# Kernel tuning notes

Measured on AMD Instinct MI355X. Metric: run time of the kernel, lower is better.

Reference implementation:

```python
import jax, jax.numpy as jnp
import numpy as np

B, S, D, H = 2, 2048, 1024, 16
DK = D // H


def setup_inputs() -> dict:
    key = jax.random.key(0)
    ks = jax.random.split(key, 8)
    Q = jax.random.normal(ks[0], (B, S, D), dtype=jnp.float32)
    K = jax.random.normal(ks[1], (B, S, D), dtype=jnp.float32)
    V = jax.random.normal(ks[2], (B, S, D), dtype=jnp.float32)
    scale = 0.02
    W_q = jax.random.normal(ks[3], (D, D), dtype=jnp.float32) * scale
    W_k = jax.random.normal(ks[4], (D, D), dtype=jnp.float32) * scale
    W_v = jax.random.normal(ks[5], (D, D), dtype=jnp.float32) * scale
    W_o = jax.random.normal(ks[6], (D, D), dtype=jnp.float32) * scale
    b_q = jnp.zeros((D,), jnp.float32)
    b_k = jnp.zeros((D,), jnp.float32)
    b_v = jnp.zeros((D,), jnp.float32)
    b_o = jnp.zeros((D,), jnp.float32)
    # causal mask, broadcastable [1,1,S,S]; mask==0 positions are masked out
    mask = jnp.tril(jnp.ones((S, S), jnp.int32))[None, None, :, :]
    return dict(Q=Q, K=K, V=V, W_q=W_q, b_q=b_q, W_k=W_k, b_k=b_k,
                W_v=W_v, b_v=b_v, W_o=W_o, b_o=b_o, mask=mask)


def reference(Q, K, V, W_q, b_q, W_k, b_k, W_v, b_v, W_o, b_o, mask):
    # linear projections (torch Linear equivalent up to weight layout)
    q = Q @ W_q + b_q   # [B,S,D]
    k = K @ W_k + b_k
    v = V @ W_v + b_v
    # split heads -> [B,H,S,DK]
    q = q.reshape(B, S, H, DK).transpose(0, 2, 1, 3)
    k = k.reshape(B, S, H, DK).transpose(0, 2, 1, 3)
    v = v.reshape(B, S, H, DK).transpose(0, 2, 1, 3)
    # scaled dot-product attention with explicit [B,H,S,S] scores
    scores = jnp.einsum('bhqd,bhkd->bhqk', q, k) / jnp.sqrt(jnp.float32(DK))
    scores = jnp.where(mask == 0, jnp.float32(-1e9), scores)
    attn = jax.nn.softmax(scores, axis=-1)
    out = jnp.einsum('bhqk,bhkd->bhqd', attn, v)
    # merge heads and output projection
    out = out.transpose(0, 2, 1, 3).reshape(B, S, D)
    return out @ W_o + b_o
```

## Files before the change

### kernel.cpp

```cpp
#include <hip/hip_runtime.h>


typedef unsigned short u16;
typedef __attribute__((ext_vector_type(8))) short s8v;
typedef __attribute__((ext_vector_type(4))) float f4v;

#define S_ 2048
#define D_ 1024
#define H_ 16
#define DK_ 64

__device__ __forceinline__ u16 f2bf(float f) {
  unsigned u = __builtin_bit_cast(unsigned, f);
  u += 0x7fffu + ((u >> 16) & 1u);
  return (u16)(u >> 16);
}
__device__ __forceinline__ u16 f2bf_t(float f) {
  return (u16)(__builtin_bit_cast(unsigned, f) >> 16);
}

__device__ __forceinline__ void gld_lds16(const u16* g, u16* l) {
  __builtin_amdgcn_global_load_lds(
      (const __attribute__((address_space(1))) unsigned int*)g,
      (__attribute__((address_space(3))) unsigned int*)l, 16, 0, 0);
}

__global__ __launch_bounds__(256) void prep(
    const float* __restrict__ Q, const float* __restrict__ K, const float* __restrict__ V,
    u16* __restrict__ Qc, u16* __restrict__ Kc, u16* __restrict__ Vc,
    const float* __restrict__ W0, const float* __restrict__ W1,
    const float* __restrict__ W2, const float* __restrict__ W3,
    u16* __restrict__ T0, u16* __restrict__ T1, u16* __restrict__ T2, u16* __restrict__ T3) {
  int bid = blockIdx.x, tid = threadIdx.x;
  if (bid < 3072) {
    int z = bid >> 10, t = bid & 1023;
    const float* s = z == 0 ? Q : z == 1 ? K : V;
    u16*         d = z == 0 ? Qc : z == 1 ? Kc : Vc;
    const int n4 = (2 * S_ * D_) / 4;
    for (int idx = t * 256 + tid; idx < n4; idx += 1024 * 256) {
      float4 f = ((const float4*)s)[idx];
      unsigned lo = (unsigned)f2bf(f.x) | ((unsigned)f2bf(f.y) << 16);
      unsigned hi = (unsigned)f2bf(f.z) | ((unsigned)f2bf(f.w) << 16);
      ((uint2*)d)[idx] = make_uint2(lo, hi);
    }
  } else {
    int wb = bid - 3072;
    int z = wb >> 10, t = wb & 1023;
    const float* W = z == 0 ? W0 : z == 1 ? W1 : z == 2 ? W2 : W3;
    u16*         T = z == 0 ? T0 : z == 1 ? T1 : z == 2 ? T2 : T3;
    __shared__ float tile[32][33];
    int tx = tid & 31, ty = tid >> 5;
    int c0 = (t & 31) * 32, r0 = (t >> 5) * 32;
#pragma unroll
    for (int i = 0; i < 32; i += 8)
      tile[ty + i][tx] = W[(size_t)(r0 + ty + i) * D_ + c0 + tx];
    __syncthreads();
#pragma unroll
    for (int i = 0; i < 32; i += 8)
      T[(size_t)(c0 + ty + i) * D_ + r0 + tx] = f2bf(tile[tx][ty + i]);
  }
}

#define BK_ 64

template <int MI, int NJ, int MODE>
__device__ __forceinline__ void gemm_core(const u16* __restrict__ A, const u16* __restrict__ Bt,
                                          const float* __restrict__ bias, void* __restrict__ out,
                                          float oscale, u16* lds, int m0, int n0) {
  constexpr int BM = MI * 32;
  constexpr int BN = NJ * 32;
  u16* Al = lds;
  u16* Bl = lds + BM * BK_;
  int tid = threadIdx.x;
  int w = tid >> 6, lane = tid & 63, quad = lane >> 4, col = lane & 15;
  int wm = (w >> 1) * (MI * 16), wn = (w & 1) * (NJ * 16);
  f4v acc[MI][NJ] = {};
  const u16* Ag = A + (size_t)m0 * 1024;
  const u16* Bg = Bt + (size_t)n0 * 1024;
  int sr = tid >> 3, ss = tid & 7;

  for (int k0 = 0; k0 < 1024; k0 += BK_) {
    __syncthreads();
#pragma unroll
    for (int c = 0; c < BM / 32; ++c) {
      int r = c * 32 + sr;
      int gs = ss ^ (r & 7);
      gld_lds16(Ag + (size_t)r * 1024 + k0 + gs * 8, &Al[r * BK_ + ss * 8]);
    }
#pragma unroll
    for (int c = 0; c < BN / 32; ++c) {
      int r = c * 32 + sr;
      int gs = ss ^ (r & 7);
      gld_lds16(Bg + (size_t)r * 1024 + k0 + gs * 8, &Bl[r * BK_ + ss * 8]);
    }
    __syncthreads();
#pragma unroll
    for (int hf = 0; hf < 2; ++hf) {
      s8v af[MI], bfr[NJ];
#pragma unroll
      for (int i = 0; i < MI; ++i) {
        int row = wm + i * 16 + col;
        int sl = (hf * 4 + quad) ^ (row & 7);
        af[i] = *(const s8v*)&Al[row * BK_ + sl * 8];
      }
#pragma unroll
      for (int j = 0; j < NJ; ++j) {
        int row = wn + j * 16 + col;
        int sl = (hf * 4 + quad) ^ (row & 7);
        bfr[j] = *(const s8v*)&Bl[row * BK_ + sl * 8];
      }
#pragma unroll
      for (int i = 0; i < MI; ++i)
#pragma unroll
        for (int j = 0; j < NJ; ++j)
          acc[i][j] = __builtin_amdgcn_mfma_f32_16x16x32_bf16(af[i], bfr[j], acc[i][j], 0, 0, 0);
    }
  }

  if (MODE == 1) {
    __syncthreads();
    u16* scr = lds + w * 2304;
    int h = (n0 + wn) >> 6;
    int dkl = lane & 31, sh = (lane >> 5) * 32;
    int mg0 = m0 + wm + sh;
    int bb = mg0 >> 11, s0g = mg0 & 2047;
    u16* ob = (u16*)out + ((size_t)(bb * H_ + h) * DK_) * S_;
#pragma unroll
    for (int t = 0; t < 2; ++t) {
#pragma unroll
      for (int j2 = 2 * t; j2 < 2 * t + 2; ++j2) {
        float bv = bias[n0 + wn + j2 * 16 + col];
        int rloc = j2 * 16 + col - t * 32;
#pragma unroll
        for (int i = 0; i < MI; ++i)
#pragma unroll
          for (int r = 0; r < 4; ++r)
            scr[rloc * 72 + i * 16 + quad * 4 + r] = f2bf(acc[i][j2][r] + bv);
      }
      __builtin_amdgcn_wave_barrier();
      u16* op = ob + (size_t)(t * 32 + dkl) * S_ + s0g;
#pragma unroll
      for (int c = 0; c < 4; ++c)
        *(uint4*)&op[c * 8] = *(const uint4*)&scr[dkl * 72 + sh + c * 8];
      __builtin_amdgcn_wave_barrier();
    }
    return;
  }

#pragma unroll
  for (int i = 0; i < MI; ++i) {
#pragma unroll
    for (int j = 0; j < NJ; ++j) {
      int n = n0 + wn + j * 16 + col;
      float bb = bias[n];
#pragma unroll
      for (int r = 0; r < 4; ++r) {
        int m = m0 + wm + i * 16 + quad * 4 + r;
        float v = (acc[i][j][r] + bb) * oscale;
        if (MODE == 2) {
          ((float*)out)[(size_t)m * 1024 + n] = v;
        } else {
          int b = m >> 11, s = m & 2047, h = n >> 6, dk = n & 63;
          ((u16*)out)[((size_t)(b * H_ + h) * S_ + s) * DK_ + dk] = f2bf(v);
        }
      }
    }
  }
}

#define CEXPQ 0.18033688f

__global__ __launch_bounds__(256, 5) void gemm_qkv(
    const u16* __restrict__ A0, const u16* __restrict__ A1, const u16* __restrict__ A2,
    const u16* __restrict__ B0, const u16* __restrict__ B1, const u16* __restrict__ B2,
    const float* __restrict__ bi0, const float* __restrict__ bi1, const float* __restrict__ bi2,
    u16* __restrict__ o0, u16* __restrict__ o1, u16* __restrict__ o2) {
  __shared__ __attribute__((aligned(16))) u16 lds[128 * BK_ + 128 * BK_];
  int k = blockIdx.x;
  int s = blockIdx.y;
  if (s < 32) {
    int ty = k * 4 + (s >> 3), tx = s & 7;
    gemm_core<4, 4, 1>(A2, B2, bi2, o2, 1.0f, lds, ty * 128, tx * 128);
  } else {
    int q = s - 32;
    int g = q >> 6;
    int r = q & 63;
    int ty = k * 4 + (r >> 4), tx = r & 15;
    if (g == 0)
      gemm_core<4, 2, 0>(A0, B0, bi0, o0, CEXPQ, lds, ty * 128, tx * 64);
    else
      gemm_core<4, 2, 0>(A1, B1, bi1, o1, 1.0f, lds, ty * 128, tx * 64);
  }
}

__global__ __launch_bounds__(256) void gemm_out(const u16* __restrict__ A, const u16* __restrict__ Bt,
                                                const float* __restrict__ bias, float* __restrict__ out) {
  __shared__ __attribute__((aligned(16))) u16 lds[64 * BK_ + 32 * BK_];
  int k = blockIdx.x;
  int s = blockIdx.y;
  int ty = k * 8 + (s >> 5), tx = s & 31;
  gemm_core<2, 1, 2>(A, Bt, bias, out, 1.0f, lds, ty * 64, tx * 32);
}

#define KT_ 64

__global__ __launch_bounds__(512, 4) void attn_fused(const u16* __restrict__ qb, const u16* __restrict__ kb,
                                                     const u16* __restrict__ vtb, u16* __restrict__ ao) {
  __shared__ __attribute__((aligned(16))) u16 Kt[2][KT_ * 64];
  __shared__ __attribute__((aligned(16))) u16 Vts[2][DK_ * 64];
  __shared__ __attribute__((aligned(16))) u16 Pl[8][16 * 64];
  int xk = blockIdx.x & 7;
  int s = (blockIdx.x >> 3) + 2 * blockIdx.y;
  int pp = s & 31, half = s >> 5;
  int bh_loc = pp & 3, jj = pp >> 2;
  int J = half ? jj : 15 - jj;
  int bh = xk * 4 + bh_loc;
  int b = bh >> 4, h = bh & 15;
  int tid = threadIdx.x, w = tid >> 6, lane = tid & 63, quad = lane >> 4, col = lane & 15;
  int qmin = J * 128 + w * 16;
  int nk = (J + 1) * 128;

  const u16* Qh = qb + (size_t)bh * S_ * DK_;
  const u16* Kh = kb + (size_t)bh * S_ * DK_;
  const u16* Vh = vtb + (size_t)bh * DK_ * S_;

  s8v qf0 = *(const s8v*)(Qh + (size_t)(qmin + col) * DK_ + quad * 8);
  s8v qf1 = *(const s8v*)(Qh + (size_t)(qmin + col) * DK_ + 32 + quad * 8);

  f4v O[4] = {};
  float ls = 0.f;

  int sr = tid >> 3, ss = tid & 7;
  int gs = ss ^ (sr & 7);
  u16* kd = &Kt[0][0] + tid * 8;
  u16* vd = &Vts[0][0] + tid * 8;
  const u16* kg = Kh + (size_t)sr * DK_ + gs * 8;
  const u16* vg = Vh + (size_t)sr * S_ + gs * 8;
  u16* Plw = &Pl[w][0];
  int xr = col & 7;

  gld_lds16(kg, kd);
  gld_lds16(vg, vd);
  __syncthreads();

  int cur = 0;
  for (int kt = 0; kt < nk; kt += KT_) {
    int kn = kt + KT_;
    if (kn < nk) {
      gld_lds16(kg + (size_t)kn * DK_, kd + (cur ^ 1) * (KT_ * 64));
      gld_lds16(vg + kn, vd + (cur ^ 1) * (DK_ * 64));
    }
    if (kt <= qmin + 15) {
      const u16* Kc = &Kt[cur][0];
      const u16* Vc = &Vts[cur][0];

      f4v sc[4];
      __builtin_amdgcn_s_setprio(1);
#pragma unroll
      for (int ks = 0; ks < 4; ++ks) {
        const u16* kr = &Kc[(ks * 16 + col) * 64];
        s8v kf0 = *(const s8v*)&kr[(quad ^ xr) * 8];
        s8v kf1 = *(const s8v*)&kr[((4 + quad) ^ xr) * 8];
        f4v t = {0.f, 0.f, 0.f, 0.f};
        t = __builtin_amdgcn_mfma_f32_16x16x32_bf16(kf0, qf0, t, 0, 0, 0);
        t = __builtin_amdgcn_mfma_f32_16x16x32_bf16(kf1, qf1, t, 0, 0, 0);
        sc[ks] = t;
      }
      __builtin_amdgcn_s_setprio(0);

      bool full = (kt + KT_ - 1 <= qmin);
      int qr = qmin + col;
#pragma unroll
      for (int ks = 0; ks < 4; ++ks) {
        float p0, p1, p2, p3;
        if (full) {
          p0 = exp2f(sc[ks][0]);
          p1 = exp2f(sc[ks][1]);
          p2 = exp2f(sc[ks][2]);
          p3 = exp2f(sc[ks][3]);
        } else {
          int kbase = kt + ks * 16 + quad * 4;
          p0 = (kbase)     <= qr ? exp2f(sc[ks][0]) : 0.f;
          p1 = (kbase + 1) <= qr ? exp2f(sc[ks][1]) : 0.f;
          p2 = (kbase + 2) <= qr ? exp2f(sc[ks][2]) : 0.f;
          p3 = (kbase + 3) <= qr ? exp2f(sc[ks][3]) : 0.f;
        }
        ls += (p0 + p1) + (p2 + p3);
        unsigned w0 = (unsigned)f2bf_t(p0) | ((unsigned)f2bf_t(p1) << 16);
        unsigned w1 = (unsigned)f2bf_t(p2) | ((unsigned)f2bf_t(p3) << 16);
        int sl = (2 * ks + (quad >> 1)) ^ xr;
        *(uint2*)&Plw[col * 64 + sl * 8 + (quad & 1) * 4] = make_uint2(w0, w1);
      }
      __builtin_amdgcn_wave_barrier();

      s8v pa0 = *(const s8v*)&Plw[col * 64 + ((quad ^ xr) * 8)];
      s8v pa1 = *(const s8v*)&Plw[col * 64 + (((4 + quad) ^ xr) * 8)];
      __builtin_amdgcn_s_setprio(1);
#pragma unroll
      for (int d = 0; d < 4; ++d) {
        const u16* vr = &Vc[(d * 16 + col) * 64];
        s8v vf0 = *(const s8v*)&vr[(quad ^ xr) * 8];
        s8v vf1 = *(const s8v*)&vr[((4 + quad) ^ xr) * 8];
        O[d] = __builtin_amdgcn_mfma_f32_16x16x32_bf16(pa0, vf0, O[d], 0, 0, 0);
        O[d] = __builtin_amdgcn_mfma_f32_16x16x32_bf16(pa1, vf1, O[d], 0, 0, 0);
      }
      __builtin_amdgcn_s_setprio(0);
      __builtin_amdgcn_wave_barrier();
    }
    __syncthreads();
    cur ^= 1;
  }

  ls += __shfl_xor(ls, 16);
  ls += __shfl_xor(ls, 32);
  float inv = 1.0f / ls;
#pragma unroll
  for (int r = 0; r < 4; ++r) {
    float invm = __shfl(inv, quad * 4 + r);
    size_t row = (size_t)(b * S_ + qmin + quad * 4 + r);
#pragma unroll
    for (int d = 0; d < 4; ++d)
      ao[row * D_ + h * DK_ + d * 16 + col] = f2bf(O[d][r] * invm);
  }
}

extern "C" void kernel_launch(void* const* d_in, const int* in_sizes, int n_in,
                              void* d_out, int out_size, void* d_ws, size_t ws_size,
                              hipStream_t stream) {
  const float* Q  = (const float*)d_in[0];
  const float* K  = (const float*)d_in[1];
  const float* V  = (const float*)d_in[2];
  const float* Wq = (const float*)d_in[3];
  const float* bq = (const float*)d_in[4];
  const float* Wk = (const float*)d_in[5];
  const float* bk = (const float*)d_in[6];
  const float* Wv = (const float*)d_in[7];
  const float* bv = (const float*)d_in[8];
  const float* Wo = (const float*)d_in[9];
  const float* bo = (const float*)d_in[10];

  char* p = (char*)d_ws;
  const size_t TEN = (size_t)2 * S_ * D_ * 2;
  const size_t WT  = (size_t)D_ * D_ * 2;
  u16* Qc  = (u16*)p; p += TEN;
  u16* Kc  = (u16*)p; p += TEN;
  u16* Vc  = (u16*)p; p += TEN;
  u16* Wqt = (u16*)p; p += WT;
  u16* Wkt = (u16*)p; p += WT;
  u16* Wvt = (u16*)p; p += WT;
  u16* Wot = (u16*)p; p += WT;
  u16* qb  = (u16*)p; p += TEN;
  u16* kbf = (u16*)p; p += TEN;
  u16* vtb = (u16*)p; p += TEN;
  u16* ao  = (u16*)p; p += TEN;

  prep<<<7168, 256, 0, stream>>>(Q, K, V, Qc, Kc, Vc, Wq, Wk, Wv, Wo, Wqt, Wkt, Wvt, Wot);
  gemm_qkv<<<dim3(8, 160), 256, 0, stream>>>(Qc, Kc, Vc, Wqt, Wkt, Wvt, bq, bk, bv, qb, kbf, vtb);
  attn_fused<<<dim3(16, 2 * H_), 512, 0, stream>>>(qb, kbf, vtb, ao);
  gemm_out<<<dim3(8, 256), 256, 0, stream>>>(ao, Wot, bo, (float*)d_out);
}
```

Before: 231.6 us.

## Shrink attention blocks to 64 query rows and prefetch K/V through registers

The attention kernel now uses 256-thread blocks covering 64 query rows instead of 512 threads covering 128, with a 1024-block grid that pairs light and heavy causal tiles per head. K/V tiles are fetched into registers one stage ahead and written to LDS, replacing direct global-to-LDS loads. The per-wave skip of fully masked key tiles is gone because every tile in the shorter loop is now needed, and the P buffer swizzle is changed to cut LDS bank conflicts. The intent is better load balance and occupancy, at the cost of more K/V reloads per query row and extra register pressure.

```diff
diff --git a/kernel.cpp b/kernel.cpp
--- a/kernel.cpp
+++ b/kernel.cpp
@@ -204,21 +204,20 @@
 
 #define KT_ 64
 
-__global__ __launch_bounds__(512, 4) void attn_fused(const u16* __restrict__ qb, const u16* __restrict__ kb,
+__global__ __launch_bounds__(256, 4) void attn_fused(const u16* __restrict__ qb, const u16* __restrict__ kb,
                                                      const u16* __restrict__ vtb, u16* __restrict__ ao) {
   __shared__ __attribute__((aligned(16))) u16 Kt[2][KT_ * 64];
   __shared__ __attribute__((aligned(16))) u16 Vts[2][DK_ * 64];
-  __shared__ __attribute__((aligned(16))) u16 Pl[8][16 * 64];
-  int xk = blockIdx.x & 7;
-  int s = (blockIdx.x >> 3) + 2 * blockIdx.y;
-  int pp = s & 31, half = s >> 5;
-  int bh_loc = pp & 3, jj = pp >> 2;
-  int J = half ? jj : 15 - jj;
+  __shared__ __attribute__((aligned(16))) u16 Pl[4][16 * 64];
+  int xk = blockIdx.x;
+  int s = blockIdx.y;
+  int bh_loc = s >> 5, sb = s & 31;
+  int J = (bh_loc & 1) ? sb : 31 - sb;
   int bh = xk * 4 + bh_loc;
   int b = bh >> 4, h = bh & 15;
   int tid = threadIdx.x, w = tid >> 6, lane = tid & 63, quad = lane >> 4, col = lane & 15;
-  int qmin = J * 128 + w * 16;
-  int nk = (J + 1) * 128;
+  int qmin = J * 64 + w * 16;
+  int nk = (J + 1) * 64;
 
   const u16* Qh = qb + (size_t)bh * S_ * DK_;
   const u16* Kh = kb + (size_t)bh * S_ * DK_;
@@ -230,83 +229,104 @@
   f4v O[4] = {};
   float ls = 0.f;
 
-  int sr = tid >> 3, ss = tid & 7;
-  int gs = ss ^ (sr & 7);
-  u16* kd = &Kt[0][0] + tid * 8;
-  u16* vd = &Vts[0][0] + tid * 8;
-  const u16* kg = Kh + (size_t)sr * DK_ + gs * 8;
-  const u16* vg = Vh + (size_t)sr * S_ + gs * 8;
+  int sr = tid >> 2, ss2 = (tid & 3) * 2;
+  int g0 = (ss2 ^ (sr & 7)) * 8;
+  int g1 = ((ss2 + 1) ^ (sr & 7)) * 8;
+  const u16* kgr = Kh + (size_t)sr * DK_;
+  const u16* vgr = Vh + (size_t)sr * S_;
+  u16* kl = &Kt[0][0] + sr * 64 + ss2 * 8;
+  u16* vl = &Vts[0][0] + sr * 64 + ss2 * 8;
   u16* Plw = &Pl[w][0];
   int xr = col & 7;
-
-  gld_lds16(kg, kd);
-  gld_lds16(vg, vd);
+  int xp = (col & 7) ^ ((col >> 3) << 2);
+
+  {
+    uint4 a = *(const uint4*)(kgr + g0), bq4 = *(const uint4*)(kgr + g1);
+    uint4 c = *(const uint4*)(vgr + g0), d = *(const uint4*)(vgr + g1);
+    *(uint4*)kl = a; *(uint4*)(kl + 8) = bq4;
+    *(uint4*)vl = c; *(uint4*)(vl + 8) = d;
+  }
+  uint4 pk0, pk1, pv0, pv1;
+  if (nk > KT_) {
+    pk0 = *(const uint4*)(kgr + (size_t)KT_ * DK_ + g0);
+    pk1 = *(const uint4*)(kgr + (size_t)KT_ * DK_ + g1);
+    pv0 = *(const uint4*)(vgr + KT_ + g0);
+    pv1 = *(const uint4*)(vgr + KT_ + g1);
+  }
   __syncthreads();
 
   int cur = 0;
   for (int kt = 0; kt < nk; kt += KT_) {
     int kn = kt + KT_;
     if (kn < nk) {
-      gld_lds16(kg + (size_t)kn * DK_, kd + (cur ^ 1) * (KT_ * 64));
-      gld_lds16(vg + kn, vd + (cur ^ 1) * (DK_ * 64));
-    }
-    if (kt <= qmin + 15) {
-      const u16* Kc = &Kt[cur][0];
-      const u16* Vc = &Vts[cur][0];
-
-      f4v sc[4];
-      __builtin_amdgcn_s_setprio(1);
-#pragma unroll
-      for (int ks = 0; ks < 4; ++ks) {
-        const u16* kr = &Kc[(ks * 16 + col) * 64];
-        s8v kf0 = *(const s8v*)&kr[(quad ^ xr) * 8];
-        s8v kf1 = *(const s8v*)&kr[((4 + quad) ^ xr) * 8];
-        f4v t = {0.f, 0.f, 0.f, 0.f};
-        t = __builtin_amdgcn_mfma_f32_16x16x32_bf16(kf0, qf0, t, 0, 0, 0);
-        t = __builtin_amdgcn_mfma_f32_16x16x32_bf16(kf1, qf1, t, 0, 0, 0);
-        sc[ks] = t;
-      }
-      __builtin_amdgcn_s_setprio(0);
-
-      bool full = (kt + KT_ - 1 <= qmin);
-      int qr = qmin + col;
-#pragma unroll
-      for (int ks = 0; ks < 4; ++ks) {
-        float p0, p1, p2, p3;
-        if (full) {
-          p0 = exp2f(sc[ks][0]);
-          p1 = exp2f(sc[ks][1]);
-          p2 = exp2f(sc[ks][2]);
-          p3 = exp2f(sc[ks][3]);
-        } else {
-          int kbase = kt + ks * 16 + quad * 4;
-          p0 = (kbase)     <= qr ? exp2f(sc[ks][0]) : 0.f;
-          p1 = (kbase + 1) <= qr ? exp2f(sc[ks][1]) : 0.f;
-          p2 = (kbase + 2) <= qr ? exp2f(sc[ks][2]) : 0.f;
-          p3 = (kbase + 3) <= qr ? exp2f(sc[ks][3]) : 0.f;
-        }
-        ls += (p0 + p1) + (p2 + p3);
-        unsigned w0 = (unsigned)f2bf_t(p0) | ((unsigned)f2bf_t(p1) << 16);
-        unsigned w1 = (unsigned)f2bf_t(p2) | ((unsigned)f2bf_t(p3) << 16);
-        int sl = (2 * ks + (quad >> 1)) ^ xr;
-        *(uint2*)&Plw[col * 64 + sl * 8 + (quad & 1) * 4] = make_uint2(w0, w1);
-      }
-      __builtin_amdgcn_wave_barrier();
-
-      s8v pa0 = *(const s8v*)&Plw[col * 64 + ((quad ^ xr) * 8)];
-      s8v pa1 = *(const s8v*)&Plw[col * 64 + (((4 + quad) ^ xr) * 8)];
-      __builtin_amdgcn_s_setprio(1);
-#pragma unroll
-      for (int d = 0; d < 4; ++d) {
-        const u16* vr = &Vc[(d * 16 + col) * 64];
-        s8v vf0 = *(const s8v*)&vr[(quad ^ xr) * 8];
-        s8v vf1 = *(const s8v*)&vr[((4 + quad) ^ xr) * 8];
-        O[d] = __builtin_amdgcn_mfma_f32_16x16x32_bf16(pa0, vf0, O[d], 0, 0, 0);
-        O[d] = __builtin_amdgcn_mfma_f32_16x16x32_bf16(pa1, vf1, O[d], 0, 0, 0);
-      }
-      __builtin_amdgcn_s_setprio(0);
-      __builtin_amdgcn_wave_barrier();
-    }
+      u16* kd = kl + (cur ^ 1) * (KT_ * 64);
+      u16* vd = vl + (cur ^ 1) * (DK_ * 64);
+      *(uint4*)kd = pk0; *(uint4*)(kd + 8) = pk1;
+      *(uint4*)vd = pv0; *(uint4*)(vd + 8) = pv1;
+      int k2 = kt + 2 * KT_;
+      if (k2 < nk) {
+        pk0 = *(const uint4*)(kgr + (size_t)k2 * DK_ + g0);
+        pk1 = *(const uint4*)(kgr + (size_t)k2 * DK_ + g1);
+        pv0 = *(const uint4*)(vgr + k2 + g0);
+        pv1 = *(const uint4*)(vgr + k2 + g1);
+      }
+    }
+    const u16* Kc = &Kt[cur][0];
+    const u16* Vc = &Vts[cur][0];
+
+    f4v sc[4];
+    __builtin_amdgcn_s_setprio(1);
+#pragma unroll
+    for (int ks = 0; ks < 4; ++ks) {
+      const u16* kr = &Kc[(ks * 16 + col) * 64];
+      s8v kf0 = *(const s8v*)&kr[(quad ^ xr) * 8];
+      s8v kf1 = *(const s8v*)&kr[((4 + quad) ^ xr) * 8];
+      f4v t = {0.f, 0.f, 0.f, 0.f};
+      t = __builtin_amdgcn_mfma_f32_16x16x32_bf16(kf0, qf0, t, 0, 0, 0);
+      t = __builtin_amdgcn_mfma_f32_16x16x32_bf16(kf1, qf1, t, 0, 0, 0);
+      sc[ks] = t;
+    }
+    __builtin_amdgcn_s_setprio(0);
+
+    bool full = (kt + KT_ - 1 <= qmin);
+    int qr = qmin + col;
+#pragma unroll
+    for (int ks = 0; ks < 4; ++ks) {
+      float p0, p1, p2, p3;
+      if (full) {
+        p0 = exp2f(sc[ks][0]);
+        p1 = exp2f(sc[ks][1]);
+        p2 = exp2f(sc[ks][2]);
+        p3 = exp2f(sc[ks][3]);
+      } else {
+        int kbase = kt + ks * 16 + quad * 4;
+        p0 = (kbase)     <= qr ? exp2f(sc[ks][0]) : 0.f;
+        p1 = (kbase + 1) <= qr ? exp2f(sc[ks][1]) : 0.f;
+        p2 = (kbase + 2) <= qr ? exp2f(sc[ks][2]) : 0.f;
+        p3 = (kbase + 3) <= qr ? exp2f(sc[ks][3]) : 0.f;
+      }
+      ls += (p0 + p1) + (p2 + p3);
+      unsigned w0 = (unsigned)f2bf_t(p0) | ((unsigned)f2bf_t(p1) << 16);
+      unsigned w1 = (unsigned)f2bf_t(p2) | ((unsigned)f2bf_t(p3) << 16);
+      int sl = (2 * ks + (quad >> 1)) ^ xp;
+      *(uint2*)&Plw[col * 64 + sl * 8 + (quad & 1) * 4] = make_uint2(w0, w1);
+    }
+    __builtin_amdgcn_wave_barrier();
+
+    s8v pa0 = *(const s8v*)&Plw[col * 64 + ((quad ^ xp) * 8)];
+    s8v pa1 = *(const s8v*)&Plw[col * 64 + (((4 + quad) ^ xp) * 8)];
+    __builtin_amdgcn_s_setprio(1);
+#pragma unroll
+    for (int d = 0; d < 4; ++d) {
+      const u16* vr = &Vc[(d * 16 + col) * 64];
+      s8v vf0 = *(const s8v*)&vr[(quad ^ xr) * 8];
+      s8v vf1 = *(const s8v*)&vr[((4 + quad) ^ xr) * 8];
+      O[d] = __builtin_amdgcn_mfma_f32_16x16x32_bf16(pa0, vf0, O[d], 0, 0, 0);
+      O[d] = __builtin_amdgcn_mfma_f32_16x16x32_bf16(pa1, vf1, O[d], 0, 0, 0);
+    }
+    __builtin_amdgcn_s_setprio(0);
+    __builtin_amdgcn_wave_barrier();
+
     __syncthreads();
     cur ^= 1;
   }
@@ -356,6 +376,6 @@
 
   prep<<<7168, 256, 0, stream>>>(Q, K, V, Qc, Kc, Vc, Wq, Wk, Wv, Wo, Wqt, Wkt, Wvt, Wot);
   gemm_qkv<<<dim3(8, 160), 256, 0, stream>>>(Qc, Kc, Vc, Wqt, Wkt, Wvt, bq, bk, bv, qb, kbf, vtb);
-  attn_fused<<<dim3(16, 2 * H_), 512, 0, stream>>>(qb, kbf, vtb, ao);
+  attn_fused<<<dim3(8, 128), 256, 0, stream>>>(qb, kbf, vtb, ao);
   gemm_out<<<dim3(8, 256), 256, 0, stream>>>(ao, Wot, bo, (float*)d_out);
 }
```

After: 232.8 us. Within noise of the previous version (+0.5%).
